# Performance work log

Hardware: AMD Instinct MI355X
Metric: run time of the kernel (lower is better)

## Reference

```python
import jax, jax.numpy as jnp
import numpy as np

LRELU_SLOPE = 0.2
ACT_GAIN = np.float32(np.sqrt(2.0))  # bias_act lrelu gain in StyleGAN2


def _per_sample_conv3x3(x, w):
    """Grouped-conv-as-batch trick: per-sample 3x3 conv.
    x: [B, C, H, W], w: [B, O, C, 3, 3] -> [B, O, H, W] (padding=1)."""
    def one(xi, wi):
        return jax.lax.conv_general_dilated(
            xi[None], wi, window_strides=(1, 1), padding=[(1, 1), (1, 1)],
            dimension_numbers=('NCHW', 'OIHW', 'NCHW'))[0]
    return jax.vmap(one)(x, w)


def setup_inputs() -> dict:
    key = jax.random.key(0)
    ks = jax.random.split(key, 10)
    B, C, R, W_DIM, IMG_C = 16, 512, 64, 512, 3
    inv_sqrt_c = np.float32(1.0 / np.sqrt(W_DIM))
    return {
        'ws': jax.random.normal(ks[0], (B, 2, W_DIM), jnp.float32),
        'const': jax.random.normal(ks[1], (C, R, R), jnp.float32),
        'conv_w': jax.random.normal(ks[2], (C, C, 3, 3), jnp.float32),
        'conv_b': jnp.zeros((C,), jnp.float32),
        'conv_aff_w': jax.random.normal(ks[3], (C, W_DIM), jnp.float32) * inv_sqrt_c,
        'conv_aff_b': jnp.ones((C,), jnp.float32),
        'noise_const': jax.random.normal(ks[4], (R, R), jnp.float32),
        'noise_strength': jnp.full((1,), 0.1, jnp.float32),
        'rgb_w': jax.random.normal(ks[5], (IMG_C, C, 1, 1), jnp.float32),
        'rgb_b': jnp.zeros((IMG_C,), jnp.float32),
        'rgb_aff_w': jax.random.normal(ks[6], (C, W_DIM), jnp.float32) * inv_sqrt_c,
        'rgb_aff_b': jnp.ones((C,), jnp.float32),
    }


def reference(ws, const, conv_w, conv_b, conv_aff_w, conv_aff_b,
              noise_const, noise_strength, rgb_w, rgb_b, rgb_aff_w, rgb_aff_b):
    B = ws.shape[0]
    # const input broadcast to batch (in_channels == 0 block)
    x = jnp.broadcast_to(const[None], (B,) + const.shape)

    # --- SynthesisLayer: modulated_conv2d (demodulate=True, fused_modconv=True) ---
    s = ws[:, 0] @ conv_aff_w.T + conv_aff_b                    # [B, C] styles
    w = conv_w[None] * s[:, None, :, None, None]                # [B, O, C, 3, 3] modulate
    dcoefs = jax.lax.rsqrt(jnp.sum(jnp.square(w), axis=(2, 3, 4)) + 1e-8)  # [B, O]
    w = w * dcoefs[:, :, None, None, None]                      # demodulate
    x = _per_sample_conv3x3(x, w)                               # grouped conv trick
    x = x + noise_const[None, None] * noise_strength            # fused noise add
    x = jax.nn.leaky_relu(x + conv_b[None, :, None, None], LRELU_SLOPE) * ACT_GAIN

    # --- ToRGBLayer: modulated 1x1 conv, demodulate=False ---
    weight_gain = np.float32(1.0 / np.sqrt(conv_w.shape[1]))    # 1/sqrt(in_ch*kh*kw)
    s2 = (ws[:, 1] @ rgb_aff_w.T + rgb_aff_b) * weight_gain     # [B, C]
    img = jnp.einsum('bchw,oc,bc->bohw', x, rgb_w[:, :, 0, 0], s2)
    img = img + rgb_b[None, :, None, None]
    return x, img
```

## Files before the change

### kernel.cpp

```cpp
#include <hip/hip_runtime.h>
#include <hip/hip_bf16.h>

typedef __attribute__((ext_vector_type(8))) short short8;
typedef __attribute__((ext_vector_type(4))) float f32x4;
typedef __attribute__((ext_vector_type(16))) float f32x16;

#define LRELU_SLOPE 0.2f
#define ACT_GAIN 1.41421356237309515f
#define WG_RGB 0.04419417382415922f
#define X1(v) ((((v) >> 2) ^ ((v) >> 3)) & 1)

__device__ __forceinline__ void glds16(const short* g, short* l) {
    __builtin_amdgcn_global_load_lds(
        (const __attribute__((address_space(1))) unsigned int*)g,
        (__attribute__((address_space(3))) unsigned int*)l, 16, 0, 0);
}

__global__ void k_init(__hip_bfloat16* __restrict__ Ypad,
                       const float* __restrict__ rgb_b, float* __restrict__ img) {
    int blk = blockIdx.x, tid = threadIdx.x;
    if (blk < 1040) {
        int gslot = blk*4 + (tid >> 6);
        int b = gslot / 260;
        int cell = gslot - b*260;
        int h, w;
        if (cell < 66)       { h = 0;          w = cell; }
        else if (cell < 132) { h = 65;         w = cell - 66; }
        else if (cell < 196) { h = cell - 131; w = 0; }
        else                 { h = cell - 195; w = 65; }
        short8 z = {};
        *(short8*)((short*)Ypad + (((b*66 + h)*66) + w)*512 + (tid & 63)*8) = z;
    } else {
        int blk2 = blk - 1040;
        #pragma unroll
        for (int j = 0; j < 4; ++j) {
            int f4 = blk2*1024 + j*256 + tid;
            int b3 = f4 >> 10;
            int o3 = b3 % 3;
            float v = rgb_b[o3];
            f32x4 vv = {v, v, v, v};
            *(f32x4*)(img + f4*4) = vv;
        }
    }
}

__global__ void k_styles(const float* __restrict__ wsin,
                         const float* __restrict__ caw, const float* __restrict__ cab,
                         const float* __restrict__ raw_, const float* __restrict__ rab,
                         float* __restrict__ sbuf, float* __restrict__ s2buf) {
    int b = blockIdx.x, which = blockIdx.y;
    int tid = threadIdx.x, lane = tid & 63, wv = tid >> 6;
    const float* aw = which ? raw_ : caw;
    const float* ab = which ? rab : cab;
    float scale = which ? WG_RGB : 1.0f;
    float* op = which ? s2buf : sbuf;
    __shared__ float wsv[512];
    wsv[tid]       = wsin[(b*2 + which)*512 + tid];
    wsv[tid + 256] = wsin[(b*2 + which)*512 + tid + 256];
    __syncthreads();
    for (int c = wv; c < 512; c += 4) {
        float p = 0.f;
        #pragma unroll
        for (int kk = 0; kk < 8; ++kk)
            p += aw[c*512 + kk*64 + lane] * wsv[kk*64 + lane];
        #pragma unroll
        for (int off = 32; off; off >>= 1) p += __shfl_down(p, off, 64);
        if (lane == 0) op[b*512 + c] = (p + ab[c]) * scale;
    }
}

__global__ __launch_bounds__(256) void k_prepw(const float* __restrict__ conv_w,
                        float* __restrict__ w2sum, __hip_bfloat16* __restrict__ Abf) {
    int o = blockIdx.x, tid = threadIdx.x;
    __shared__ float wrow[4608];
    const f32x4* src = (const f32x4*)(conv_w + o*4608);
    #pragma unroll
    for (int r = 0; r < 5; ++r) {
        int idx = tid + (r << 8);
        if (idx < 1152) *(f32x4*)&wrow[idx*4] = src[idx];
    }
    __syncthreads();
    #pragma unroll
    for (int j = 0; j < 2; ++j) {
        int c = tid + (j << 8);
        float sum = 0.f;
        #pragma unroll
        for (int t = 0; t < 9; ++t) {
            float v = wrow[c*9 + t];
            sum += v*v;
            Abf[(t*512 + o)*512 + c] = __float2bfloat16(v);
        }
        w2sum[o*512 + c] = sum;
    }
}

__global__ __launch_bounds__(256) void k_dcoef(const float* __restrict__ sbuf,
                                               const float* __restrict__ w2sum,
                                               const float* __restrict__ s2buf,
                                               const float* __restrict__ rgb_w,
                                               float* __restrict__ dcoef,
                                               float* __restrict__ rgbc) {
    int gw = blockIdx.x*4 + (threadIdx.x >> 6);
    int lane = threadIdx.x & 63;
    int b = gw >> 9, o = gw & 511;
    float acc = 0.f;
    #pragma unroll
    for (int i = 0; i < 8; ++i) {
        int c = (i << 6) + lane;
        float sv = sbuf[(b << 9) + c];
        acc += sv*sv*w2sum[(o << 9) + c];
    }
    #pragma unroll
    for (int off = 32; off; off >>= 1) acc += __shfl_down(acc, off, 64);
    if (lane == 0) dcoef[(b << 9) + o] = rsqrtf(acc + 1e-8f);
    if (blockIdx.x < 96) {
        int flat = blockIdx.x*256 + threadIdx.x;
        int bb = flat / 1536;
        int r  = flat - bb*1536;
        int c  = r & 511;
        rgbc[flat] = rgb_w[r] * s2buf[bb*512 + c];
    }
}

__global__ void k_ypad(const float* __restrict__ cst, const float* __restrict__ sbuf,
                       __hip_bfloat16* __restrict__ Ypad) {
    int b = blockIdx.x >> 6, h = blockIdx.x & 63, tid = threadIdx.x;
    __shared__ float tile[64][65];
    for (int cc = 0; cc < 8; ++cc) {
        int c0 = cc << 6;
        #pragma unroll
        for (int it = 0; it < 16; ++it) {
            int cl = (it << 2) + (tid >> 6);
            int w = tid & 63;
            tile[cl][w] = cst[(c0 + cl)*4096 + (h << 6) + w];
        }
        __syncthreads();
        #pragma unroll
        for (int it = 0; it < 16; ++it) {
            int flat = (it << 8) + tid;
            int w = flat >> 6, cl = flat & 63;
            float v = sbuf[(b << 9) + c0 + cl] * tile[cl][w];
            Ypad[(((b*66 + h + 1)*66) + (w + 1))*512 + c0 + cl] = __float2bfloat16(v);
        }
        __syncthreads();
    }
}

__global__ __launch_bounds__(512, 2) void conv_gemm(
    const short* __restrict__ Abf,
    const short* __restrict__ Ypad,
    const float* __restrict__ dcoef,
    const float* __restrict__ noise,
    const float* __restrict__ nstr,
    const float* __restrict__ bias,
    const float* __restrict__ rgbc,
    float* __restrict__ xout,
    float* __restrict__ img)
{
    __shared__ short SH[59392];
    short* Aring = SH;
    short* Bbuf  = SH + 32768;
    float (*red)[3][2] = (float (*)[3][2])SH;

    int tid = threadIdx.x, lane = tid & 63, wv = tid >> 6;
    int wr = wv >> 2, wc = wv & 3;
    int ml32 = lane & 31, hi = lane >> 5;

    int blk = blockIdx.x;
    int xcd = blk & 7, idx = blk >> 3;
    int v = xcd * 64 + idx;
    int mblk = v & 1, nblk = v >> 1;
    int b = nblk >> 4;
    int hw0 = (nblk & 15) << 8;
    int h0 = hw0 >> 6;
    int o0 = mblk << 8;

    int bsrc[3];
    #pragma unroll
    for (int r = 0; r < 3; ++r) {
        int j = tid + (r << 9);
        int ks = (j >= 832) ? 1 : 0;
        int pe = (j - ks*832) >> 1;
        int pos = pe > 395 ? 395 : pe;
        int half = j & 1;
        int q = half ^ X1(pos);
        int hl = pos / 66, ww = pos - hl*66;
        bsrc[r] = (((b*66 + h0 + hl)*66) + ww)*512 + ks*16 + q*8;
    }
    int bsrc3;
    {
        int j = 1536 + wv*16 + (lane & 15);
        int pe = (j - 832) >> 1;
        int pos = pe > 395 ? 395 : pe;
        int half = j & 1;
        int q = half ^ X1(pos);
        int hl = pos / 66, ww = pos - hl*66;
        bsrc3 = (((b*66 + h0 + hl)*66) + ww)*512 + 16 + q*8;
    }
    int agofs[2];
    #pragma unroll
    for (int r = 0; r < 2; ++r) {
        int row = tid >> 1, half = tid & 1;
        int q = half ^ X1(row);
        agofs[r] = ((o0 + row) << 9) + r*16 + q*8;
    }
    int aro[4];
    #pragma unroll
    for (int mi = 0; mi < 4; ++mi) {
        int row = wr*128 + mi*32 + ml32;
        aro[mi] = row*16 + ((hi ^ X1(row)) << 3);
    }
    int pb0 = wc*66 + ml32;
    const int BPA[9] = {0, 1, 2, 66, 67, 68, 132, 133, 134};

    short* AW = Aring + wv*512;

    f32x16 acc[4][2] = {};
    short8 faA[4], fbA[2], faB[4], fbB[2];

    #pragma unroll
    for (int r = 0; r < 3; ++r)
        glds16(Ypad + bsrc[r], Bbuf + wv*512 + r*4096);
    if ((lane & 63) < 16) glds16(Ypad + bsrc3, Bbuf + 12288 + wv*128);
    #pragma unroll
    for (int t = 0; t < 3; ++t) {
        glds16(Abf + (t << 18) + agofs[0], AW + t*8192);
        glds16(Abf + (t << 18) + agofs[1], AW + t*8192 + 4096);
    }
    asm volatile("s_waitcnt vmcnt(2)" ::: "memory");
    __builtin_amdgcn_s_barrier();
    #pragma unroll
    for (int mi = 0; mi < 4; ++mi)
        faA[mi] = *(const short8*)(Aring + aro[mi]);
    #pragma unroll
    for (int ni = 0; ni < 2; ++ni) {
        int p_ = pb0 + ni*32;
        fbA[ni] = *(const short8*)(Bbuf + p_*16 + ((hi ^ X1(p_)) << 3));
    }

    constexpr int VMP[9] = {3, 3, 3, 3, 2, 2, 2, 2, 2};

#define MMCL(FA, FB)                                                        \
    __builtin_amdgcn_s_setprio(1);                                          \
    _Pragma("unroll")                                                       \
    for (int mi = 0; mi < 4; ++mi)                                          \
        _Pragma("unroll")                                                   \
        for (int ni = 0; ni < 2; ++ni)                                      \
            acc[mi][ni] = __builtin_amdgcn_mfma_f32_32x32x16_bf16(          \
                FA[mi], FB[ni], acc[mi][ni], 0, 0, 0);                      \
    __builtin_amdgcn_s_setprio(0);

#define PH(TAP)                                                             \
    {                                                                       \
        int rr  = (rb + (TAP)) & 3;                                         \
        int rrN = (rb + (TAP) + 1) & 3;                                     \
        int rw  = (rb + (TAP) + 3) & 3;                                     \
        constexpr int TAPN = ((TAP) + 1) % 9;                               \
        constexpr int TAPP = ((TAP) < 6) ? (TAP) + 3 : (TAP) - 6;           \
                                            \
        _Pragma("unroll")                                                   \
        for (int mi = 0; mi < 4; ++mi)                                      \
            faB[mi] = *(const short8*)(Aring + rr*8192 + 4096 + aro[mi]);   \
        _Pragma("unroll")                                                   \
        for (int ni = 0; ni < 2; ++ni) {                                    \
            int p_ = pb0 + BPA[(TAP)] + ni*32;                              \
            fbB[ni] = *(const short8*)(Bcur + 6656 + p_*16                  \
                                       + ((hi ^ X1(p_)) << 3));             \
        }                                                                   \
             \
        { const short* asrc_ = Abf + (TAPP << 18) + (((TAP) < 6) ? c0 : c0n); \
          glds16(asrc_ + agofs[0], AW + rw*8192);                           \
          glds16(asrc_ + agofs[1], AW + rw*8192 + 4096); }                  \
        if ((TAP) < 3) glds16(Ypad + bsrc[(TAP)] + c0n, BWn + (TAP)*4096);  \
        if ((TAP) == 3) { if ((lane & 63) < 16)                             \
            glds16(Ypad + bsrc3 + c0n, BRm); }                              \
        __builtin_amdgcn_sched_barrier(0);                                  \
        MMCL(faA, fbA)                                                      \
        __builtin_amdgcn_sched_barrier(0);                                  \
                                                  \
        { const short* BbN = ((TAP) == 8) ? Bnxt : Bcur;                    \
          _Pragma("unroll")                                                 \
          for (int mi = 0; mi < 4; ++mi)                                    \
              faA[mi] = *(const short8*)(Aring + rrN*8192 + aro[mi]);       \
          _Pragma("unroll")                                                 \
          for (int ni = 0; ni < 2; ++ni) {                                  \
              int p_ = pb0 + BPA[TAPN] + ni*32;                             \
              fbA[ni] = *(const short8*)(BbN + p_*16                        \
                                         + ((hi ^ X1(p_)) << 3));           \
          } }                                                               \
        __builtin_amdgcn_sched_barrier(0);                                  \
        MMCL(faB, fbB)                                                      \
        asm volatile("s_waitcnt vmcnt(%0)" :: "i"(VMP[(TAP)]) : "memory");  \
        __builtin_amdgcn_s_barrier();                                       \
    }

    for (int ch = 0; ch < 16; ++ch) {
        int c0 = ch << 5;
        int c0n = (c0 + 32) & 511;
        int rb = ch & 3;
        int half = ch & 1;
        const short* Bcur = Bbuf + half*13312;
        const short* Bnxt = Bbuf + (half ^ 1)*13312;
        short* BWn = (short*)Bnxt + wv*512;
        short* BRm = (short*)Bnxt + 12288 + wv*128;
        PH(0) PH(1) PH(2) PH(3) PH(4) PH(5) PH(6) PH(7) PH(8)
    }
#undef PH
#undef MMCL

    asm volatile("s_waitcnt vmcnt(0)" ::: "memory");
    __builtin_amdgcn_s_barrier();

    float ns = nstr[0];
    float pr0[2] = {0.f, 0.f}, pr1[2] = {0.f, 0.f}, pr2[2] = {0.f, 0.f};
    #pragma unroll
    for (int mi = 0; mi < 4; ++mi) {
        int ob = o0 + wr*128 + mi*32 + hi*4;
        f32x4 dc[4], bs[4], c0r[4], c1r[4], c2r[4];
        #pragma unroll
        for (int g = 0; g < 4; ++g) {
            dc[g]  = *(const f32x4*)(dcoef + (b << 9) + ob + g*8);
            bs[g]  = *(const f32x4*)(bias + ob + g*8);
            c0r[g] = *(const f32x4*)(rgbc + b*1536 + ob + g*8);
            c1r[g] = *(const f32x4*)(rgbc + b*1536 + 512 + ob + g*8);
            c2r[g] = *(const f32x4*)(rgbc + b*1536 + 1024 + ob + g*8);
        }
        #pragma unroll
        for (int ni = 0; ni < 2; ++ni) {
            int nl = wc*64 + ni*32 + ml32;
            int hw = hw0 + nl;
            float nz = noise[hw] * ns;
            #pragma unroll
            for (int g = 0; g < 4; ++g)
                #pragma unroll
                for (int t = 0; t < 4; ++t) {
                    float vv = acc[mi][ni][g*4 + t] * dc[g][t] + nz + bs[g][t];
                    vv = (vv < 0.f ? LRELU_SLOPE*vv : vv) * ACT_GAIN;
                    xout[(((b << 9) + ob + g*8 + t) << 12) + hw] = vv;
                    pr0[ni] += vv * c0r[g][t];
                    pr1[ni] += vv * c1r[g][t];
                    pr2[ni] += vv * c2r[g][t];
                }
        }
    }
    #pragma unroll
    for (int ni = 0; ni < 2; ++ni) {
        pr0[ni] += __shfl_down(pr0[ni], 32, 64);
        pr1[ni] += __shfl_down(pr1[ni], 32, 64);
        pr2[ni] += __shfl_down(pr2[ni], 32, 64);
    }
    if (lane < 32) {
        #pragma unroll
        for (int ni = 0; ni < 2; ++ni) {
            int nl = wc*64 + ni*32 + ml32;
            red[nl][0][wr] = pr0[ni];
            red[nl][1][wr] = pr1[ni];
            red[nl][2][wr] = pr2[ni];
        }
    }
    __syncthreads();
    for (int p = tid; p < 768; p += 512) {
        int o3 = p >> 8, nl = p & 255;
        atomicAdd(img + ((b*3 + o3) << 12) + hw0 + nl, red[nl][o3][0] + red[nl][o3][1]);
    }
}

extern "C" void kernel_launch(void* const* d_in, const int* in_sizes, int n_in,
                              void* d_out, int out_size, void* d_ws, size_t ws_size,
                              hipStream_t stream) {
    (void)in_sizes; (void)n_in; (void)out_size; (void)ws_size;
    const float* wsin   = (const float*)d_in[0];
    const float* cst    = (const float*)d_in[1];
    const float* conv_w = (const float*)d_in[2];
    const float* conv_b = (const float*)d_in[3];
    const float* caw    = (const float*)d_in[4];
    const float* cab    = (const float*)d_in[5];
    const float* noise  = (const float*)d_in[6];
    const float* nstr   = (const float*)d_in[7];
    const float* rgb_w  = (const float*)d_in[8];
    const float* rgb_b  = (const float*)d_in[9];
    const float* raw_   = (const float*)d_in[10];
    const float* rab    = (const float*)d_in[11];

    char* wsb = (char*)d_ws;
    float* sbuf   = (float*)(wsb + 0);
    float* s2buf  = (float*)(wsb + 32768);
    float* dcoef  = (float*)(wsb + 65536);
    float* rgbc   = (float*)(wsb + 98304);
    float* w2sum  = (float*)(wsb + 196608);
    __hip_bfloat16* Abf  = (__hip_bfloat16*)(wsb + 1245184);
    __hip_bfloat16* Ypad = (__hip_bfloat16*)(wsb + 5963776);

    float* xout = (float*)d_out;
    float* img  = xout + 33554432;

    k_init<<<1088, 256, 0, stream>>>(Ypad, rgb_b, img);
    k_styles<<<dim3(16, 2), 256, 0, stream>>>(wsin, caw, cab, raw_, rab, sbuf, s2buf);
    k_prepw<<<512, 256, 0, stream>>>(conv_w, w2sum, Abf);
    k_dcoef<<<2048, 256, 0, stream>>>(sbuf, w2sum, s2buf, rgb_w, dcoef, rgbc);
    k_ypad<<<1024, 256, 0, stream>>>(cst, sbuf, Ypad);
    conv_gemm<<<512, 512, 0, stream>>>((const short*)Abf, (const short*)Ypad,
                                       dcoef, noise, nstr, conv_b, rgbc, xout, img);
}
```

Before: 572.9 us.

## Merge prep kernels into two launches, vectorize Ypad stores, add LDS waits

Five independent preprocessing kernels become two, using block-index ranges: init, styles and weight prep in one; dcoef/rgbc and the padded modulated input in the other. This cuts launch gaps and serialization between the small kernels. The Ypad writer now packs 8 bf16 channels into one 16-byte store, where before each thread stored a single bf16. In the GEMM main loop, explicit lgkmcnt waits are placed before each MFMA cluster, which changes how LDS fragment loads overlap with the MFMAs.

Result: slower. 589.3 us (+2.9%).

```diff
diff --git a/kernel.cpp b/kernel.cpp
--- a/kernel.cpp
+++ b/kernel.cpp
@@ -16,133 +16,144 @@
         (__attribute__((address_space(3))) unsigned int*)l, 16, 0, 0);
 }
 
-__global__ void k_init(__hip_bfloat16* __restrict__ Ypad,
-                       const float* __restrict__ rgb_b, float* __restrict__ img) {
+__global__ __launch_bounds__(256) void k_pre1(
+    __hip_bfloat16* __restrict__ Ypad, const float* __restrict__ rgb_b,
+    float* __restrict__ img, const float* __restrict__ wsin,
+    const float* __restrict__ caw, const float* __restrict__ cab,
+    const float* __restrict__ raw_, const float* __restrict__ rab,
+    float* __restrict__ sbuf, float* __restrict__ s2buf,
+    const float* __restrict__ conv_w, float* __restrict__ w2sum,
+    __hip_bfloat16* __restrict__ Abf) {
+    __shared__ float shf[4608];
     int blk = blockIdx.x, tid = threadIdx.x;
-    if (blk < 1040) {
-        int gslot = blk*4 + (tid >> 6);
-        int b = gslot / 260;
-        int cell = gslot - b*260;
-        int h, w;
-        if (cell < 66)       { h = 0;          w = cell; }
-        else if (cell < 132) { h = 65;         w = cell - 66; }
-        else if (cell < 196) { h = cell - 131; w = 0; }
-        else                 { h = cell - 195; w = 65; }
-        short8 z = {};
-        *(short8*)((short*)Ypad + (((b*66 + h)*66) + w)*512 + (tid & 63)*8) = z;
+    if (blk < 1088) {
+        if (blk < 1040) {
+            int gslot = blk*4 + (tid >> 6);
+            int b = gslot / 260;
+            int cell = gslot - b*260;
+            int h, w;
+            if (cell < 66)       { h = 0;          w = cell; }
+            else if (cell < 132) { h = 65;         w = cell - 66; }
+            else if (cell < 196) { h = cell - 131; w = 0; }
+            else                 { h = cell - 195; w = 65; }
+            short8 z = {};
+            *(short8*)((short*)Ypad + (((b*66 + h)*66) + w)*512 + (tid & 63)*8) = z;
+        } else {
+            int blk2 = blk - 1040;
+            #pragma unroll
+            for (int j = 0; j < 4; ++j) {
+                int f4 = blk2*1024 + j*256 + tid;
+                int b3 = f4 >> 10;
+                int o3 = b3 % 3;
+                float v = rgb_b[o3];
+                f32x4 vv = {v, v, v, v};
+                *(f32x4*)(img + f4*4) = vv;
+            }
+        }
+    } else if (blk < 1120) {
+        int idx = blk - 1088;
+        int b = idx >> 1, which = idx & 1;
+        int lane = tid & 63, wv = tid >> 6;
+        const float* aw = which ? raw_ : caw;
+        const float* ab = which ? rab : cab;
+        float scale = which ? WG_RGB : 1.0f;
+        float* op = which ? s2buf : sbuf;
+        float* wsv = shf;
+        wsv[tid]       = wsin[(b*2 + which)*512 + tid];
+        wsv[tid + 256] = wsin[(b*2 + which)*512 + tid + 256];
+        __syncthreads();
+        for (int c = wv; c < 512; c += 4) {
+            float p = 0.f;
+            #pragma unroll
+            for (int kk = 0; kk < 8; ++kk)
+                p += aw[c*512 + kk*64 + lane] * wsv[kk*64 + lane];
+            #pragma unroll
+            for (int off = 32; off; off >>= 1) p += __shfl_down(p, off, 64);
+            if (lane == 0) op[b*512 + c] = (p + ab[c]) * scale;
+        }
     } else {
-        int blk2 = blk - 1040;
-        #pragma unroll
-        for (int j = 0; j < 4; ++j) {
-            int f4 = blk2*1024 + j*256 + tid;
-            int b3 = f4 >> 10;
-            int o3 = b3 % 3;
-            float v = rgb_b[o3];
-            f32x4 vv = {v, v, v, v};
-            *(f32x4*)(img + f4*4) = vv;
+        int o = blk - 1120;
+        float* wrow = shf;
+        const f32x4* src = (const f32x4*)(conv_w + o*4608);
+        #pragma unroll
+        for (int r = 0; r < 5; ++r) {
+            int idx = tid + (r << 8);
+            if (idx < 1152) *(f32x4*)&wrow[idx*4] = src[idx];
+        }
+        __syncthreads();
+        #pragma unroll
+        for (int j = 0; j < 2; ++j) {
+            int c = tid + (j << 8);
+            float sum = 0.f;
+            #pragma unroll
+            for (int t = 0; t < 9; ++t) {
+                float v = wrow[c*9 + t];
+                sum += v*v;
+                Abf[(t*512 + o)*512 + c] = __float2bfloat16(v);
+            }
+            w2sum[o*512 + c] = sum;
         }
     }
 }
 
-__global__ void k_styles(const float* __restrict__ wsin,
-                         const float* __restrict__ caw, const float* __restrict__ cab,
-                         const float* __restrict__ raw_, const float* __restrict__ rab,
-                         float* __restrict__ sbuf, float* __restrict__ s2buf) {
-    int b = blockIdx.x, which = blockIdx.y;
-    int tid = threadIdx.x, lane = tid & 63, wv = tid >> 6;
-    const float* aw = which ? raw_ : caw;
-    const float* ab = which ? rab : cab;
-    float scale = which ? WG_RGB : 1.0f;
-    float* op = which ? s2buf : sbuf;
-    __shared__ float wsv[512];
-    wsv[tid]       = wsin[(b*2 + which)*512 + tid];
-    wsv[tid + 256] = wsin[(b*2 + which)*512 + tid + 256];
-    __syncthreads();
-    for (int c = wv; c < 512; c += 4) {
-        float p = 0.f;
-        #pragma unroll
-        for (int kk = 0; kk < 8; ++kk)
-            p += aw[c*512 + kk*64 + lane] * wsv[kk*64 + lane];
-        #pragma unroll
-        for (int off = 32; off; off >>= 1) p += __shfl_down(p, off, 64);
-        if (lane == 0) op[b*512 + c] = (p + ab[c]) * scale;
-    }
-}
-
-__global__ __launch_bounds__(256) void k_prepw(const float* __restrict__ conv_w,
-                        float* __restrict__ w2sum, __hip_bfloat16* __restrict__ Abf) {
-    int o = blockIdx.x, tid = threadIdx.x;
-    __shared__ float wrow[4608];
-    const f32x4* src = (const f32x4*)(conv_w + o*4608);
-    #pragma unroll
-    for (int r = 0; r < 5; ++r) {
-        int idx = tid + (r << 8);
-        if (idx < 1152) *(f32x4*)&wrow[idx*4] = src[idx];
-    }
-    __syncthreads();
-    #pragma unroll
-    for (int j = 0; j < 2; ++j) {
-        int c = tid + (j << 8);
-        float sum = 0.f;
-        #pragma unroll
-        for (int t = 0; t < 9; ++t) {
-            float v = wrow[c*9 + t];
-            sum += v*v;
-            Abf[(t*512 + o)*512 + c] = __float2bfloat16(v);
-        }
-        w2sum[o*512 + c] = sum;
-    }
-}
-
-__global__ __launch_bounds__(256) void k_dcoef(const float* __restrict__ sbuf,
-                                               const float* __restrict__ w2sum,
-                                               const float* __restrict__ s2buf,
-                                               const float* __restrict__ rgb_w,
-                                               float* __restrict__ dcoef,
-                                               float* __restrict__ rgbc) {
-    int gw = blockIdx.x*4 + (threadIdx.x >> 6);
-    int lane = threadIdx.x & 63;
-    int b = gw >> 9, o = gw & 511;
-    float acc = 0.f;
-    #pragma unroll
-    for (int i = 0; i < 8; ++i) {
-        int c = (i << 6) + lane;
-        float sv = sbuf[(b << 9) + c];
-        acc += sv*sv*w2sum[(o << 9) + c];
-    }
-    #pragma unroll
-    for (int off = 32; off; off >>= 1) acc += __shfl_down(acc, off, 64);
-    if (lane == 0) dcoef[(b << 9) + o] = rsqrtf(acc + 1e-8f);
-    if (blockIdx.x < 96) {
-        int flat = blockIdx.x*256 + threadIdx.x;
-        int bb = flat / 1536;
-        int r  = flat - bb*1536;
-        int c  = r & 511;
-        rgbc[flat] = rgb_w[r] * s2buf[bb*512 + c];
-    }
-}
-
-__global__ void k_ypad(const float* __restrict__ cst, const float* __restrict__ sbuf,
-                       __hip_bfloat16* __restrict__ Ypad) {
-    int b = blockIdx.x >> 6, h = blockIdx.x & 63, tid = threadIdx.x;
+__global__ __launch_bounds__(256) void k_pre2(
+    const float* __restrict__ sbuf, const float* __restrict__ w2sum,
+    const float* __restrict__ s2buf, const float* __restrict__ rgb_w,
+    float* __restrict__ dcoef, float* __restrict__ rgbc,
+    const float* __restrict__ cst, __hip_bfloat16* __restrict__ Ypad) {
     __shared__ float tile[64][65];
-    for (int cc = 0; cc < 8; ++cc) {
-        int c0 = cc << 6;
-        #pragma unroll
-        for (int it = 0; it < 16; ++it) {
-            int cl = (it << 2) + (tid >> 6);
-            int w = tid & 63;
-            tile[cl][w] = cst[(c0 + cl)*4096 + (h << 6) + w];
-        }
-        __syncthreads();
-        #pragma unroll
-        for (int it = 0; it < 16; ++it) {
-            int flat = (it << 8) + tid;
-            int w = flat >> 6, cl = flat & 63;
-            float v = sbuf[(b << 9) + c0 + cl] * tile[cl][w];
-            Ypad[(((b*66 + h + 1)*66) + (w + 1))*512 + c0 + cl] = __float2bfloat16(v);
-        }
-        __syncthreads();
+    __shared__ float sv[64];
+    int blk = blockIdx.x, tid = threadIdx.x;
+    if (blk < 2048) {
+        int gw = blk*4 + (tid >> 6);
+        int lane = tid & 63;
+        int b = gw >> 9, o = gw & 511;
+        float acc = 0.f;
+        #pragma unroll
+        for (int i = 0; i < 8; ++i) {
+            int c = (i << 6) + lane;
+            float svv = sbuf[(b << 9) + c];
+            acc += svv*svv*w2sum[(o << 9) + c];
+        }
+        #pragma unroll
+        for (int off = 32; off; off >>= 1) acc += __shfl_down(acc, off, 64);
+        if (lane == 0) dcoef[(b << 9) + o] = rsqrtf(acc + 1e-8f);
+        if (blk < 96) {
+            int flat = blk*256 + tid;
+            int bb = flat / 1536;
+            int r  = flat - bb*1536;
+            int c  = r & 511;
+            rgbc[flat] = rgb_w[r] * s2buf[bb*512 + c];
+        }
+    } else {
+        int blk2 = blk - 2048;
+        int b = blk2 >> 6, h = blk2 & 63;
+        for (int cc = 0; cc < 8; ++cc) {
+            int c0 = cc << 6;
+            #pragma unroll
+            for (int it = 0; it < 16; ++it) {
+                int cl = (it << 2) + (tid >> 6);
+                int w = tid & 63;
+                tile[cl][w] = cst[(c0 + cl)*4096 + (h << 6) + w];
+            }
+            if (tid < 64) sv[tid] = sbuf[(b << 9) + c0 + tid];
+            __syncthreads();
+            #pragma unroll
+            for (int it = 0; it < 2; ++it) {
+                int u = (it << 8) + tid;
+                int w = u >> 3, cg = u & 7;
+                short8 v;
+                #pragma unroll
+                for (int j = 0; j < 8; ++j) {
+                    float f = sv[cg*8 + j] * tile[cg*8 + j][w];
+                    __hip_bfloat16 bf = __float2bfloat16(f);
+                    v[j] = reinterpret_cast<short&>(bf);
+                }
+                *(short8*)((short*)Ypad + (((b*66 + h + 1)*66) + (w + 1))*512
+                           + c0 + cg*8) = v;
+            }
+            __syncthreads();
+        }
     }
 }
 
@@ -257,7 +268,7 @@
         int rw  = (rb + (TAP) + 3) & 3;                                     \
         constexpr int TAPN = ((TAP) + 1) % 9;                               \
         constexpr int TAPP = ((TAP) < 6) ? (TAP) + 3 : (TAP) - 6;           \
-                                            \
+                                 \
         _Pragma("unroll")                                                   \
         for (int mi = 0; mi < 4; ++mi)                                      \
             faB[mi] = *(const short8*)(Aring + rr*8192 + 4096 + aro[mi]);   \
@@ -275,9 +286,12 @@
         if ((TAP) == 3) { if ((lane & 63) < 16)                             \
             glds16(Ypad + bsrc3 + c0n, BRm); }                              \
         __builtin_amdgcn_sched_barrier(0);                                  \
+                   \
+        asm volatile("s_waitcnt lgkmcnt(6)" ::: "memory");                  \
+        __builtin_amdgcn_sched_barrier(0);                                  \
         MMCL(faA, fbA)                                                      \
         __builtin_amdgcn_sched_barrier(0);                                  \
-                                                  \
+                                       \
         { const short* BbN = ((TAP) == 8) ? Bnxt : Bcur;                    \
           _Pragma("unroll")                                                 \
           for (int mi = 0; mi < 4; ++mi)                                    \
@@ -288,6 +302,9 @@
               fbA[ni] = *(const short8*)(BbN + p_*16                        \
                                          + ((hi ^ X1(p_)) << 3));           \
           } }                                                               \
+        __builtin_amdgcn_sched_barrier(0);                                  \
+                        \
+        asm volatile("s_waitcnt lgkmcnt(6)" ::: "memory");                  \
         __builtin_amdgcn_sched_barrier(0);                                  \
         MMCL(faB, fbB)                                                      \
         asm volatile("s_waitcnt vmcnt(%0)" :: "i"(VMP[(TAP)]) : "memory");  \
@@ -394,11 +411,10 @@
     float* xout = (float*)d_out;
     float* img  = xout + 33554432;
 
-    k_init<<<1088, 256, 0, stream>>>(Ypad, rgb_b, img);
-    k_styles<<<dim3(16, 2), 256, 0, stream>>>(wsin, caw, cab, raw_, rab, sbuf, s2buf);
-    k_prepw<<<512, 256, 0, stream>>>(conv_w, w2sum, Abf);
-    k_dcoef<<<2048, 256, 0, stream>>>(sbuf, w2sum, s2buf, rgb_w, dcoef, rgbc);
-    k_ypad<<<1024, 256, 0, stream>>>(cst, sbuf, Ypad);
+    k_pre1<<<1632, 256, 0, stream>>>(Ypad, rgb_b, img, wsin, caw, cab, raw_, rab,
+                                     sbuf, s2buf, conv_w, w2sum, Abf);
+    k_pre2<<<3072, 256, 0, stream>>>(sbuf, w2sum, s2buf, rgb_w, dcoef, rgbc,
+                                     cst, Ypad);
     conv_gemm<<<512, 512, 0, stream>>>((const short*)Abf, (const short*)Ypad,
                                        dcoef, noise, nstr, conv_b, rgbc, xout, img);
 }
```
